# Optimization experiments

Hardware: AMD Instinct MI355X
Metric: run time of the kernel (lower is better)

Reference implementation:

```python
import jax, jax.numpy as jnp
import numpy as np

WD, WH, WW = 6, 6, 6
NUM_HEADS = 8
EPS = 1e-5


def setup_inputs() -> dict:
    key = jax.random.key(0)
    ks = jax.random.split(key, 4)
    B, C, D, H, W = 1, 128, 48, 48, 48
    return {
        "q_map": jax.random.normal(ks[0], (B, C, D, H, W), dtype=jnp.float32),
        "k_map": jax.random.normal(ks[1], (B, C, D, H, W), dtype=jnp.float32),
        "v_map": jax.random.normal(ks[2], (B, C, D, H, W), dtype=jnp.float32),
        "gamma_q": jnp.ones((C,), jnp.float32),
        "beta_q": jnp.zeros((C,), jnp.float32),
        "gamma_kv": jnp.ones((C,), jnp.float32),
        "beta_kv": jnp.zeros((C,), jnp.float32),
        "proj_w": jax.random.normal(ks[3], (C, C), dtype=jnp.float32) * (1.0 / np.sqrt(C)),
        "proj_b": jnp.zeros((C,), jnp.float32),
    }


def _layernorm(x, g, b):
    m = jnp.mean(x, axis=-1, keepdims=True)
    v = jnp.mean(jnp.square(x - m), axis=-1, keepdims=True)
    return (x - m) * jax.lax.rsqrt(v + EPS) * g + b


def _window_partition(x):
    # x: (B, D, H, W, C) -> windows: (B*nD*nH*nW, wd*wh*ww, C)
    B, D, H, W, C = x.shape
    pd, ph, pw = (WD - D % WD) % WD, (WH - H % WH) % WH, (WW - W % WW) % WW
    if pd or ph or pw:
        x = jnp.pad(x, ((0, 0), (0, pd), (0, ph), (0, pw), (0, 0)))
    Dp, Hp, Wp = D + pd, H + ph, W + pw
    x = x.reshape(B, Dp // WD, WD, Hp // WH, WH, Wp // WW, WW, C)
    x = jnp.transpose(x, (0, 1, 3, 5, 2, 4, 6, 7))
    return x.reshape(-1, WD * WH * WW, C), (D, H, W, Dp, Hp, Wp)


def _window_reverse(windows, meta):
    D, H, W, Dp, Hp, Wp = meta
    C = windows.shape[-1]
    nD, nH, nW = Dp // WD, Hp // WH, Wp // WW
    B = windows.shape[0] // (nD * nH * nW)
    x = windows.reshape(B, nD, nH, nW, WD, WH, WW, C)
    x = jnp.transpose(x, (0, 1, 4, 2, 5, 3, 6, 7)).reshape(B, Dp, Hp, Wp, C)
    return x[:, :D, :H, :W, :]


def reference(q_map, k_map, v_map, gamma_q, beta_q, gamma_kv, beta_kv, proj_w, proj_b):
    # (B, C, D, H, W) -> (B, D, H, W, C)
    q_map = jnp.transpose(q_map, (0, 2, 3, 4, 1))
    k_map = jnp.transpose(k_map, (0, 2, 3, 4, 1))
    v_map = jnp.transpose(v_map, (0, 2, 3, 4, 1))

    q, meta = _window_partition(q_map)
    k, _ = _window_partition(k_map)
    v, _ = _window_partition(v_map)

    q = _layernorm(q, gamma_q, beta_q)
    k = _layernorm(k, gamma_kv, beta_kv)
    v = _layernorm(v, gamma_kv, beta_kv)

    Bw, Nq, C = q.shape
    dh = C // NUM_HEADS
    q = q.reshape(Bw, Nq, NUM_HEADS, dh)
    k = k.reshape(Bw, -1, NUM_HEADS, dh)
    v = v.reshape(Bw, -1, NUM_HEADS, dh)

    scale = 1.0 / np.sqrt(dh).astype(np.float32)
    scores = jnp.einsum("bqhd,bkhd->bhqk", q, k) * scale  # (Bw, h, Nq, Nk)
    attn = jax.nn.softmax(scores, axis=-1)
    out = jnp.einsum("bhqk,bkhd->bqhd", attn, v).reshape(Bw, Nq, C)

    out = out @ proj_w.T + proj_b
    out = _window_reverse(out, meta)
    return jnp.transpose(out, (0, 4, 1, 2, 3))  # (B, C, D, H, W)
```

## Files before the change

### kernel.cpp

```cpp
#include <hip/hip_runtime.h>
#include <hip/hip_bf16.h>

typedef short s16x8 __attribute__((ext_vector_type(8)));
typedef float f32x2 __attribute__((ext_vector_type(2)));
typedef float f32x4 __attribute__((ext_vector_type(4)));
typedef float f32x16 __attribute__((ext_vector_type(16)));
typedef unsigned int u32;
typedef unsigned short u16;
typedef u32 u32x4v __attribute__((ext_vector_type(4)));

#define TOK 216
#define T1 448
#define SP 110592
#define BUF0 0
#define VOFF 57344
#define WOFF 122880
#define GBOFF 155648
#define LDS_OLD 157696
#define VHOFF 28672
#define TENB 28311552ull
#define WSNEED (3ull*TENB + 32768ull)
#define QSCALE 0.360673760f

__device__ __forceinline__ u32 pack2(float a, float b) {
  u16 lo = __builtin_bit_cast(u16, __float2bfloat16(a));
  u16 hi = __builtin_bit_cast(u16, __float2bfloat16(b));
  return (u32)lo | ((u32)hi << 16);
}
__device__ __forceinline__ int swz(int row, int inner) {
  return inner ^ ((row & 7) << 4);
}
__device__ __forceinline__ void gload16(const void* g, void* l) {
  __builtin_amdgcn_global_load_lds(
      (const __attribute__((address_space(1))) void*)g,
      (__attribute__((address_space(3))) void*)l, 16, 0, 0);
}

__device__ __forceinline__ void ln_stats(const f32x2* xv, float& mA, float& rA,
                                         float& mB, float& rB) {
  float sA = 0.f, s2A = 0.f, sB = 0.f, s2B = 0.f;
#pragma unroll
  for (int c = 0; c < 32; ++c) {
    sA += xv[c].x; s2A += xv[c].x * xv[c].x;
    sB += xv[c].y; s2B += xv[c].y * xv[c].y;
  }
  sA += __shfl_xor(sA, 1); s2A += __shfl_xor(s2A, 1);
  sB += __shfl_xor(sB, 1); s2B += __shfl_xor(s2B, 1);
  sA += __shfl_xor(sA, 2); s2A += __shfl_xor(s2A, 2);
  sB += __shfl_xor(sB, 2); s2B += __shfl_xor(s2B, 2);
  mA = sA * (1.0f / 128.0f);
  rA = rsqrtf(s2A * (1.0f / 128.0f) - mA * mA + 1e-5f);
  mB = sB * (1.0f / 128.0f);
  rB = rsqrtf(s2B * (1.0f / 128.0f) - mB * mB + 1e-5f);
}

template<bool MASK>
__device__ __forceinline__ void attn_stepH(const char* smem, int jloc, int kt,
                                           s16x8 qfh, int lane,
                                           f32x16& acc, float& lsum) {
  const int half = lane >> 5;
  const int krow = kt * 32 + (lane & 31);
  s16x8 kf = *(const s16x8*)(smem + krow * 128 +
                             ((jloc * 32 + half * 16) ^ ((krow & 7) << 4)));
  f32x16 st = __builtin_amdgcn_mfma_f32_32x32x16_bf16(kf, qfh, (f32x16){}, 0, 0, 0);
  const int vrow = jloc * 16 + (lane & 15);
  s16x8 vf0 = *(const s16x8*)(smem + VHOFF + vrow * 512 +
                              ((kt * 64 + half * 16) ^ ((vrow & 7) << 4)));
  s16x8 vf1 = *(const s16x8*)(smem + VHOFF + vrow * 512 +
                              ((kt * 64 + 32 + half * 16) ^ ((vrow & 7) << 4)));
  const int NR = MASK ? 12 : 16;
  u32 A[8];
  float ts0 = 0.f, ts1 = 0.f;
#pragma unroll
  for (int i = 0; i < 8; ++i) {
    float p0 = (2 * i < NR) ? __builtin_amdgcn_exp2f(st[2 * i]) : 0.f;
    float p1 = (2 * i + 1 < NR) ? __builtin_amdgcn_exp2f(st[2 * i + 1]) : 0.f;
    if (i & 1) ts1 += p0 + p1; else ts0 += p0 + p1;
    A[i] = pack2(p0, p1);
  }
  lsum += ts0 + ts1;
  s16x8 pf0 = __builtin_bit_cast(s16x8, (u32x4v){A[0], A[1], A[2], A[3]});
  s16x8 pf1 = __builtin_bit_cast(s16x8, (u32x4v){A[4], A[5], A[6], A[7]});
  acc = __builtin_amdgcn_mfma_f32_32x32x16_bf16(vf0, pf0, acc, 0, 0, 0);
  acc = __builtin_amdgcn_mfma_f32_32x32x16_bf16(vf1, pf1, acc, 0, 0, 0);
}

template<bool MASK>
__device__ __forceinline__ void attn_stepF(const char* smem, int h, int kt,
                                           s16x8 qfh, int lane,
                                           f32x16& acc, float& lsum) {
  const int half = lane >> 5;
  const int krow = kt * 32 + (lane & 31);
  s16x8 kf = *(const s16x8*)(smem + BUF0 + krow * 256 +
                             swz(krow, h * 32 + half * 16));
  f32x16 st = __builtin_amdgcn_mfma_f32_32x32x16_bf16(kf, qfh, (f32x16){}, 0, 0, 0);
  const int vrow = h * 16 + (lane & 15);
  s16x8 vf0 = *(const s16x8*)(smem + VOFF + vrow * 512 +
                              swz(vrow, kt * 64 + half * 16));
  s16x8 vf1 = *(const s16x8*)(smem + VOFF + vrow * 512 +
                              swz(vrow, kt * 64 + 32 + half * 16));
  const int NR = MASK ? 12 : 16;
  u32 A[8];
  float ts0 = 0.f, ts1 = 0.f;
#pragma unroll
  for (int i = 0; i < 8; ++i) {
    float p0 = (2 * i < NR) ? __builtin_amdgcn_exp2f(st[2 * i]) : 0.f;
    float p1 = (2 * i + 1 < NR) ? __builtin_amdgcn_exp2f(st[2 * i + 1]) : 0.f;
    if (i & 1) ts1 += p0 + p1; else ts0 += p0 + p1;
    A[i] = pack2(p0, p1);
  }
  lsum += ts0 + ts1;
  s16x8 pf0 = __builtin_bit_cast(s16x8, (u32x4v){A[0], A[1], A[2], A[3]});
  s16x8 pf1 = __builtin_bit_cast(s16x8, (u32x4v){A[4], A[5], A[6], A[7]});
  acc = __builtin_amdgcn_mfma_f32_32x32x16_bf16(vf0, pf0, acc, 0, 0, 0);
  acc = __builtin_amdgcn_mfma_f32_32x32x16_bf16(vf1, pf1, acc, 0, 0, 0);
}

extern "C" __global__ __launch_bounds__(256)
void lnpre_kernel(const float* __restrict__ qm, const float* __restrict__ km,
                  const float* __restrict__ vm,
                  const float* __restrict__ gq, const float* __restrict__ bq,
                  const float* __restrict__ gkv, const float* __restrict__ bkv,
                  const float* __restrict__ pw,
                  u16* __restrict__ qn, u16* __restrict__ kn,
                  u16* __restrict__ vn, u16* __restrict__ wbf) {
  const int tid = threadIdx.x;
  const int bid = blockIdx.x;
  if (bid >= 6912) {
#pragma unroll
    for (int k = 0; k < 32; ++k) {
      int idx = tid + 256 * k;
      f32x2 w2 = *(const f32x2*)(pw + idx * 2);
      ((u32*)wbf)[idx] = pack2(w2.x, w2.y);
    }
    return;
  }
  __shared__ __align__(16) float lf[6144];
  __shared__ float gl[128], bl[128];
  const int t = bid / 2304, idx = bid - t * 2304;
  const float* src = t == 0 ? qm : (t == 1 ? km : vm);
  u16* dst = t == 0 ? qn : (t == 1 ? kn : vn);
  const float* gsrc = (t == 0) ? gq : gkv;
  const float* bsrc = (t == 0) ? bq : bkv;
  const float scale = (t == 0) ? QSCALE : 1.0f;
  const int d = idx / 48, h = idx - d * 48;
  const int dh = d * 2304 + h * 48;
  const int lane = tid & 63, wv = tid >> 6;

  if (tid < 128) { gl[tid] = gsrc[tid]; bl[tid] = bsrc[tid]; }
  for (int uu = wv; uu < 24; uu += 4) {
    int j = uu * 64 + lane;
    int ch = j / 12, wq = j - ch * 12;
    gload16(src + (long)ch * SP + dh + wq * 4, (char*)lf + uu * 1024);
  }
  __syncthreads();

  if (tid < 192) {
    const int w = tid >> 2, q = tid & 3;
    float s = 0.f, s2 = 0.f;
#pragma unroll
    for (int c = 0; c < 32; ++c) {
      float x = lf[(q + 4 * c) * 48 + w];
      s += x; s2 += x * x;
    }
    s += __shfl_xor(s, 1); s2 += __shfl_xor(s2, 1);
    s += __shfl_xor(s, 2); s2 += __shfl_xor(s2, 2);
    float m = s * (1.f / 128.f);
    float r = rsqrtf(s2 * (1.f / 128.f) - m * m + 1e-5f);
    u32x4v* op = (u32x4v*)(dst + (long)(dh + w) * 128 + 32 * q);
#pragma unroll
    for (int v4 = 0; v4 < 4; ++v4) {
      u32x4v pk;
#pragma unroll
      for (int e = 0; e < 4; ++e) {
        int ch = 32 * q + v4 * 8 + 2 * e;
        float y0 = ((lf[ch * 48 + w] - m) * r * gl[ch] + bl[ch]) * scale;
        float y1 = ((lf[(ch + 1) * 48 + w] - m) * r * gl[ch + 1] + bl[ch + 1]) * scale;
        pk[e] = pack2(y0, y1);
      }
      op[v4] = pk;
    }
  }
}

extern "C" __global__ __launch_bounds__(448, 4)
void attnh_kernel(u16* __restrict__ qn, const u16* __restrict__ kn,
                  const u16* __restrict__ vn) {
  __shared__ __align__(16) char smem[61440];
  const int tid = threadIdx.x, lane = tid & 63, wv = tid >> 6;
  const int half = lane >> 5;
  const int bid = blockIdx.x;
  const int wid = bid >> 1, hg = bid & 1;
  const int wd6 = (wid >> 6) * 6, wh6 = ((wid >> 3) & 7) * 6, ww6 = (wid & 7) * 6;

  for (int uu = wv; uu < 27; uu += 7) {
    int row = 8 * uu + (lane >> 3);
    int tq = row / 6;
    int g = (wd6 + tq / 6) * 2304 + (wh6 + tq % 6) * 48 + ww6 + row % 6;
    gload16(kn + g * 128 + hg * 64 + (((lane & 7) ^ (row & 7)) << 3),
            smem + uu * 1024);
  }
  for (int uu = wv; uu < 27; uu += 7) {
    int row = 8 * uu + (lane >> 3);
    int tq = row / 6;
    int g = (wd6 + tq / 6) * 2304 + (wh6 + tq % 6) * 48 + ww6 + row % 6;
    gload16(vn + g * 128 + hg * 64 + ((lane & 7) << 3),
            smem + VHOFF + uu * 1024);
  }
  int qrow = wv * 32 + (lane & 31);
  if (qrow > 215) qrow = 215;
  int qtq = qrow / 6;
  int qg = (wd6 + qtq / 6) * 2304 + (wh6 + qtq % 6) * 48 + ww6 + qrow % 6;
  s16x8 qf[4];
#pragma unroll
  for (int j = 0; j < 4; ++j)
    qf[j] = *(const s16x8*)(qn + qg * 128 + (hg * 4 + j) * 16 + half * 8);
  __syncthreads();

  u32 tr[16];
#pragma unroll
  for (int k = 0; k < 8; ++k) {
    int u = tid + 448 * k;
    if (u < 3456) {
      int t = (u >> 5) * 2, c2 = u & 31;
      tr[2 * k]     = *(const u32*)(smem + VHOFF + t * 128 + c2 * 4);
      tr[2 * k + 1] = *(const u32*)(smem + VHOFF + t * 128 + 128 + c2 * 4);
    }
  }
  __syncthreads();
#pragma unroll
  for (int k = 0; k < 8; ++k) {
    int u = tid + 448 * k;
    if (u < 3456) {
      int t = (u >> 5) * 2, c2 = u & 31;
      int st = (t & ~12) | ((t & 4) << 1) | ((t & 8) >> 1);
      int c = 2 * c2;
      u32 w0 = (tr[2 * k] & 0xFFFFu) | (tr[2 * k + 1] << 16);
      u32 w1 = (tr[2 * k] >> 16) | (tr[2 * k + 1] & 0xFFFF0000u);
      *(u32*)(smem + VHOFF + c * 512 + ((st * 2) ^ ((c & 7) << 4))) = w0;
      *(u32*)(smem + VHOFF + (c + 1) * 512 + ((st * 2) ^ (((c + 1) & 7) << 4))) = w1;
    }
  }
  if (tid < 64) {
    int x = (tid & 7) << 4;
    *(u32*)(smem + VHOFF + tid * 512 + (424 ^ x)) = 0;
    *(u32*)(smem + VHOFF + tid * 512 + (428 ^ x)) = 0;
    *(u32*)(smem + VHOFF + tid * 512 + (440 ^ x)) = 0;
    *(u32*)(smem + VHOFF + tid * 512 + (444 ^ x)) = 0;
  }
  __syncthreads();

  u32 oPk[4][4];
#pragma unroll
  for (int hp = 0; hp < 2; ++hp) {
    const int j0 = 2 * hp, j1 = j0 + 1;
    f32x16 a0 = {}, a1 = {};
    float l0 = 0.f, l1 = 0.f;
#pragma unroll 2
    for (int kt = 0; kt < 6; ++kt) {
      attn_stepH<false>(smem, j0, kt, qf[j0], lane, a0, l0);
      attn_stepH<false>(smem, j1, kt, qf[j1], lane, a1, l1);
    }
    attn_stepH<true>(smem, j0, 6, qf[j0], lane, a0, l0);
    attn_stepH<true>(smem, j1, 6, qf[j1], lane, a1, l1);
    l0 += __shfl_xor(l0, 32);
    l1 += __shfl_xor(l1, 32);
    float i0 = 1.0f / l0, i1 = 1.0f / l1;
#pragma unroll
    for (int r = 0; r < 4; ++r) {
      oPk[j0][r] = pack2(a0[2 * r] * i0, a0[2 * r + 1] * i0);
      oPk[j1][r] = pack2(a1[2 * r] * i1, a1[2 * r + 1] * i1);
    }
  }
  __syncthreads();

  {
    const int tok = wv * 32 + (lane & 31);
#pragma unroll
    for (int j = 0; j < 4; ++j) {
      int chb = j * 32 + half * 8;
      *(u32*)(smem + tok * 128 + ((chb)      ^ ((tok & 7) << 4))) = oPk[j][0];
      *(u32*)(smem + tok * 128 + ((chb + 4)  ^ ((tok & 7) << 4))) = oPk[j][1];
      *(u32*)(smem + tok * 128 + ((chb + 16) ^ ((tok & 7) << 4))) = oPk[j][2];
      *(u32*)(smem + tok * 128 + ((chb + 20) ^ ((tok & 7) << 4))) = oPk[j][3];
    }
  }
  __syncthreads();

#pragma unroll
  for (int it = 0; it < 4; ++it) {
    int i = tid + 448 * it;
    int row = i >> 3;
    if (row < 216) {
      int chunk = i & 7;
      f32x4 v = *(const f32x4*)(smem + row * 128 +
                                ((chunk * 16) ^ ((row & 7) << 4)));
      int tq = row / 6;
      int g = (wd6 + tq / 6) * 2304 + (wh6 + tq % 6) * 48 + ww6 + row % 6;
      *(f32x4*)(qn + g * 128 + hg * 64 + chunk * 8) = v;
    }
  }
}

extern "C" __global__ __launch_bounds__(256, 3)
void proj_kernel(const u16* __restrict__ on, const u16* __restrict__ wbf,
                 const float* __restrict__ pb, float* __restrict__ out) {
  __shared__ __align__(16) char smem[45056];
  const int tid = threadIdx.x, lane = tid & 63, wv = tid >> 6;
  const int bid = blockIdx.x;
  const int dh = (bid / 48) * 2304 + (bid % 48) * 48;
  for (int uu = wv; uu < 32; uu += 4) {
    int row = 4 * uu + (lane >> 4);
    gload16(wbf + row * 128 + (((lane & 15) ^ (row & 15)) << 3),
            smem + uu * 1024);
  }
  for (int uu = wv; uu < 12; uu += 4) {
    int row = 4 * uu + (lane >> 4);
    gload16(on + (long)(dh + row) * 128 + (((lane & 15) ^ (row & 15)) << 3),
            smem + 32768 + uu * 1024);
  }
  __syncthreads();
#pragma unroll
  for (int jj = 0; jj < 2; ++jj) {
    int jt = wv * 2 + jj;
    int rw = jt * 16 + (lane & 15);
    s16x8 af[4];
#pragma unroll
    for (int kk = 0; kk < 4; ++kk)
      af[kk] = *(const s16x8*)(smem + rw * 256 +
                               ((kk * 64 + (lane >> 4) * 16) ^ ((rw & 15) << 4)));
    f32x4 pbv = *(const f32x4*)(pb + jt * 16 + (lane >> 4) * 4);
#pragma unroll
    for (int t = 0; t < 3; ++t) {
      int tok = t * 16 + (lane & 15);
      f32x4 acc = {};
#pragma unroll
      for (int kk = 0; kk < 4; ++kk) {
        s16x8 bfr = *(const s16x8*)(smem + 32768 + tok * 256 +
                                    ((kk * 64 + (lane >> 4) * 16) ^ ((tok & 15) << 4)));
        acc = __builtin_amdgcn_mfma_f32_16x16x32_bf16(af[kk], bfr, acc, 0, 0, 0);
      }
#pragma unroll
      for (int r = 0; r < 4; ++r) {
        int j = jt * 16 + (lane >> 4) * 4 + r;
        out[(long)j * SP + dh + tok] = acc[r] + pbv[r];
      }
    }
  }
}

extern "C" __global__ __launch_bounds__(T1, 2)
void ca3d_kernel(const float* __restrict__ qm, const float* __restrict__ km,
                 const float* __restrict__ vm,
                 const float* __restrict__ gq, const float* __restrict__ bq,
                 const float* __restrict__ gkv, const float* __restrict__ bkv,
                 const float* __restrict__ pw, const float* __restrict__ pb,
                 float* __restrict__ out) {
  extern __shared__ __align__(16) char smem[];
  const int tid = threadIdx.x;
  const int lane = tid & 63;
  const int wv = tid >> 6;
  const int bid = blockIdx.x;
  const int wid = ((bid & 7) << 6) | (bid >> 3);
  const int wd = wid >> 6, wh = (wid >> 3) & 7, ww = wid & 7;
  const int boff = wd * 6 * 2304 + wh * 6 * 48 + ww * 6;

  for (int i = tid * 16; i < VOFF + 65536; i += T1 * 16)
    *(f32x4*)(smem + i) = (f32x4){};
  if (tid < 128) {
    ((float*)(smem + GBOFF))[tid] = gq[tid];
    ((float*)(smem + GBOFF + 512))[tid] = bq[tid];
    ((float*)(smem + GBOFF + 1024))[tid] = gkv[tid];
    ((float*)(smem + GBOFF + 1536))[tid] = bkv[tid];
  }
  const bool lnAct = tid < 432;
  const int tp = tid >> 2;
  const int cbase = (tid & 3) * 32;
  const int tA = tp * 2, tB = tA + 1;
  int td = tA / 36, tr_ = tA - td * 36;
  int th_ = tr_ / 6, tw_ = tr_ - th_ * 6;
  const int gpos = boff + td * 2304 + th_ * 48 + tw_;
  const int vposA = (tA & ~0xC) | ((tA & 4) << 1) | ((tA & 8) >> 1);

  f32x2 qv[32], kv[32], vv[32];
  if (lnAct) {
#pragma unroll
    for (int c = 0; c < 32; ++c)
      qv[c] = *(const f32x2*)(qm + gpos + (cbase + c) * SP);
#pragma unroll
    for (int c = 0; c < 32; ++c)
      kv[c] = *(const f32x2*)(km + gpos + (cbase + c) * SP);
  }
  __syncthreads();
  const float* gql = (const float*)(smem + GBOFF);
  const float* bql = (const float*)(smem + GBOFF + 512);
  const float* gkl = (const float*)(smem + GBOFF + 1024);
  const float* bkl = (const float*)(smem + GBOFF + 1536);
  if (lnAct) {
    float mA, rA, mB, rB;
    ln_stats(qv, mA, rA, mB, rB);
#pragma unroll
    for (int c = 0; c < 32; c += 2) {
      int cc = cbase + c;
      float g0 = gql[cc], g1 = gql[cc + 1], b0 = bql[cc], b1 = bql[cc + 1];
      *(u32*)(smem + BUF0 + tA * 256 + swz(tA, cc * 2)) =
          pack2(((qv[c].x - mA) * rA * g0 + b0) * QSCALE,
                ((qv[c + 1].x - mA) * rA * g1 + b1) * QSCALE);
      *(u32*)(smem + BUF0 + tB * 256 + swz(tB, cc * 2)) =
          pack2(((qv[c].y - mB) * rB * g0 + b0) * QSCALE,
                ((qv[c + 1].y - mB) * rB * g1 + b1) * QSCALE);
    }
#pragma unroll
    for (int c = 0; c < 32; ++c)
      vv[c] = *(const f32x2*)(vm + gpos + (cbase + c) * SP);
  }
  __syncthreads();
  s16x8 qf[8];
  {
    int row = wv * 32 + (lane & 31);
    int ib = (lane >> 5) * 16;
#pragma unroll
    for (int h = 0; h < 8; ++h)
      qf[h] = *(const s16x8*)(smem + BUF0 + row * 256 + swz(row, h * 32 + ib));
  }
  __syncthreads();
  if (lnAct) {
    {
      float mA, rA, mB, rB;
      ln_stats(kv, mA, rA, mB, rB);
#pragma unroll
      for (int c = 0; c < 32; c += 2) {
        int cc = cbase + c;
        float g0 = gkl[cc], g1 = gkl[cc + 1], b0 = bkl[cc], b1 = bkl[cc + 1];
        *(u32*)(smem + BUF0 + tA * 256 + swz(tA, cc * 2)) =
            pack2((kv[c].x - mA) * rA * g0 + b0,
                  (kv[c + 1].x - mA) * rA * g1 + b1);
        *(u32*)(smem + BUF0 + tB * 256 + swz(tB, cc * 2)) =
            pack2((kv[c].y - mB) * rB * g0 + b0,
                  (kv[c + 1].y - mB) * rB * g1 + b1);
      }
    }
    {
      float mA, rA, mB, rB;
      ln_stats(vv, mA, rA, mB, rB);
#pragma unroll
      for (int c = 0; c < 32; ++c) {
        int cc = cbase + c;
        float g0 = gkl[cc], b0 = bkl[cc];
        *(u32*)(smem + VOFF + cc * 512 + swz(cc, vposA * 2)) =
            pack2((vv[c].x - mA) * rA * g0 + b0,
                  (vv[c].y - mB) * rB * g0 + b0);
      }
    }
  }
  for (int i = tid; i < 8192; i += T1) {
    int j = i >> 6, c2 = i & 63;
    f32x2 w2 = *(const f32x2*)(pw + j * 128 + c2 * 2);
    *(u32*)(smem + WOFF + j * 256 + swz(j, c2 * 4)) = pack2(w2.x, w2.y);
  }
  __syncthreads();
  u32 oPk[8][4];
#pragma unroll
  for (int hp = 0; hp < 4; ++hp) {
    const int h0 = hp * 2, h1 = h0 + 1;
    f32x16 a0 = {}, a1 = {};
    float l0 = 0.f, l1 = 0.f;
#pragma unroll 1
    for (int kt = 0; kt < 6; ++kt) {
      attn_stepF<false>(smem, h0, kt, qf[h0], lane, a0, l0);
      attn_stepF<false>(smem, h1, kt, qf[h1], lane, a1, l1);
    }
    attn_stepF<true>(smem, h0, 6, qf[h0], lane, a0, l0);
    attn_stepF<true>(smem, h1, 6, qf[h1], lane, a1, l1);
    l0 += __shfl_xor(l0, 32);
    l1 += __shfl_xor(l1, 32);
    float i0 = 1.0f / l0, i1 = 1.0f / l1;
#pragma unroll
    for (int r = 0; r < 4; ++r) {
      oPk[h0][r] = pack2(a0[2 * r] * i0, a0[2 * r + 1] * i0);
      oPk[h1][r] = pack2(a1[2 * r] * i1, a1[2 * r + 1] * i1);
    }
  }
  __syncthreads();
  {
    const int tok = wv * 32 + (lane & 31);
    const int half = lane >> 5;
#pragma unroll
    for (int h = 0; h < 8; ++h) {
      int chb = h * 32 + half * 8;
      *(u32*)(smem + BUF0 + tok * 256 + swz(tok, chb))      = oPk[h][0];
      *(u32*)(smem + BUF0 + tok * 256 + swz(tok, chb + 4))  = oPk[h][1];
      *(u32*)(smem + BUF0 + tok * 256 + swz(tok, chb + 16)) = oPk[h][2];
      *(u32*)(smem + BUF0 + tok * 256 + swz(tok, chb + 20)) = oPk[h][3];
    }
  }
  __syncthreads();
#pragma unroll 1
  for (int ti = 0; ti < 2; ++ti) {
    int tt = wv * 2 + ti;
    int tok = tt * 16 + (lane & 15);
    s16x8 bfr[4];
#pragma unroll
    for (int kk = 0; kk < 4; ++kk)
      bfr[kk] = *(const s16x8*)(smem + BUF0 + tok * 256 +
                                swz(tok, kk * 64 + (lane >> 4) * 16));
    bool tokValid = tok < TOK;
    int tdd = tok / 36, trr = tok - tdd * 36;
    int thh = trr / 6, tww = trr - thh * 6;
    int pos = boff + tdd * 2304 + thh * 48 + tww;
#pragma unroll 1
    for (int jt = 0; jt < 8; ++jt) {
      f32x4 acc = {};
#pragma unroll
      for (int kk = 0; kk < 4; ++kk) {
        int rw = jt * 16 + (lane & 15);
        s16x8 af = *(const s16x8*)(smem + WOFF + rw * 256 +
                                   swz(rw, kk * 64 + (lane >> 4) * 16));
        acc = __builtin_amdgcn_mfma_f32_16x16x32_bf16(af, bfr[kk], acc, 0, 0, 0);
      }
      f32x4 pbv = *(const f32x4*)(pb + jt * 16 + (lane >> 4) * 4);
      if (tokValid) {
#pragma unroll
        for (int r = 0; r < 4; ++r) {
          int j = jt * 16 + (lane >> 4) * 4 + r;
          out[j * SP + pos] = acc[r] + pbv[r];
        }
      }
    }
  }
}

extern "C" void kernel_launch(void* const* d_in, const int* in_sizes, int n_in,
                              void* d_out, int out_size, void* d_ws, size_t ws_size,
                              hipStream_t stream) {
  const float* qm  = (const float*)d_in[0];
  const float* km  = (const float*)d_in[1];
  const float* vm  = (const float*)d_in[2];
  const float* gq  = (const float*)d_in[3];
  const float* bq  = (const float*)d_in[4];
  const float* gkv = (const float*)d_in[5];
  const float* bkv = (const float*)d_in[6];
  const float* pw  = (const float*)d_in[7];
  const float* pb  = (const float*)d_in[8];
  if (ws_size >= WSNEED) {
    u16* qn  = (u16*)d_ws;
    u16* kn  = (u16*)((char*)d_ws + TENB);
    u16* vn  = (u16*)((char*)d_ws + 2 * TENB);
    u16* wbf = (u16*)((char*)d_ws + 3 * TENB);
    hipLaunchKernelGGL(lnpre_kernel, dim3(6913), dim3(256), 0, stream,
                       qm, km, vm, gq, bq, gkv, bkv, pw, qn, kn, vn, wbf);
    hipLaunchKernelGGL(attnh_kernel, dim3(1024), dim3(448), 0, stream,
                       qn, kn, vn);
    hipLaunchKernelGGL(proj_kernel, dim3(2304), dim3(256), 0, stream,
                       qn, wbf, pb, (float*)d_out);
  } else {
    hipLaunchKernelGGL(ca3d_kernel, dim3(512), dim3(T1), LDS_OLD, stream,
                       qm, km, vm, gq, bq, gkv, bkv, pw, pb, (float*)d_out);
  }
}
```

Baseline: 137.0 us.

## Restructure layernorm prepass to per-token register reduction with swizzled LDS transpose

The layernorm prepass is rewritten so that each wave owns 64 consecutive tokens and each lane reduces one token across all 128 channels directly from global memory, replacing the cooperative LDS staging and cross-lane shuffle reduction. The normalized values are packed to bf16, written to a per-wave XOR-swizzled LDS tile, and then stored coalesced in token-major layout. Block count and size drop to 2593 blocks of 128 threads. The input is read twice (once for the statistics, once for normalization), which relies on cache hits and trades extra load traffic for simpler indexing and fewer barriers.

```diff
diff --git a/kernel.cpp b/kernel.cpp
--- a/kernel.cpp
+++ b/kernel.cpp
@@ -116,7 +116,7 @@
   acc = __builtin_amdgcn_mfma_f32_32x32x16_bf16(vf1, pf1, acc, 0, 0, 0);
 }
 
-extern "C" __global__ __launch_bounds__(256)
+extern "C" __global__ __launch_bounds__(128)
 void lnpre_kernel(const float* __restrict__ qm, const float* __restrict__ km,
                   const float* __restrict__ vm,
                   const float* __restrict__ gq, const float* __restrict__ bq,
@@ -126,60 +126,63 @@
                   u16* __restrict__ vn, u16* __restrict__ wbf) {
   const int tid = threadIdx.x;
   const int bid = blockIdx.x;
-  if (bid >= 6912) {
-#pragma unroll
-    for (int k = 0; k < 32; ++k) {
-      int idx = tid + 256 * k;
+  if (bid >= 2592) {
+#pragma unroll
+    for (int k = 0; k < 64; ++k) {
+      int idx = tid + 128 * k;
       f32x2 w2 = *(const f32x2*)(pw + idx * 2);
       ((u32*)wbf)[idx] = pack2(w2.x, w2.y);
     }
     return;
   }
-  __shared__ __align__(16) float lf[6144];
-  __shared__ float gl[128], bl[128];
-  const int t = bid / 2304, idx = bid - t * 2304;
+  __shared__ __align__(16) char lds[32768];
+  const int lane = tid & 63, wv = tid >> 6;
+  const int t = bid / 864, rb = bid - t * 864;
   const float* src = t == 0 ? qm : (t == 1 ? km : vm);
   u16* dst = t == 0 ? qn : (t == 1 ? kn : vn);
-  const float* gsrc = (t == 0) ? gq : gkv;
-  const float* bsrc = (t == 0) ? bq : bkv;
+  const float* g = (t == 0) ? gq : gkv;
+  const float* b = (t == 0) ? bq : bkv;
   const float scale = (t == 0) ? QSCALE : 1.0f;
-  const int d = idx / 48, h = idx - d * 48;
-  const int dh = d * 2304 + h * 48;
-  const int lane = tid & 63, wv = tid >> 6;
-
-  if (tid < 128) { gl[tid] = gsrc[tid]; bl[tid] = bsrc[tid]; }
-  for (int uu = wv; uu < 24; uu += 4) {
-    int j = uu * 64 + lane;
-    int ch = j / 12, wq = j - ch * 12;
-    gload16(src + (long)ch * SP + dh + wq * 4, (char*)lf + uu * 1024);
-  }
-  __syncthreads();
-
-  if (tid < 192) {
-    const int w = tid >> 2, q = tid & 3;
-    float s = 0.f, s2 = 0.f;
-#pragma unroll
-    for (int c = 0; c < 32; ++c) {
-      float x = lf[(q + 4 * c) * 48 + w];
-      s += x; s2 += x * x;
-    }
-    s += __shfl_xor(s, 1); s2 += __shfl_xor(s2, 1);
-    s += __shfl_xor(s, 2); s2 += __shfl_xor(s2, 2);
-    float m = s * (1.f / 128.f);
-    float r = rsqrtf(s2 * (1.f / 128.f) - m * m + 1e-5f);
-    u32x4v* op = (u32x4v*)(dst + (long)(dh + w) * 128 + 32 * q);
-#pragma unroll
-    for (int v4 = 0; v4 < 4; ++v4) {
-      u32x4v pk;
-#pragma unroll
-      for (int e = 0; e < 4; ++e) {
-        int ch = 32 * q + v4 * 8 + 2 * e;
-        float y0 = ((lf[ch * 48 + w] - m) * r * gl[ch] + bl[ch]) * scale;
-        float y1 = ((lf[(ch + 1) * 48 + w] - m) * r * gl[ch + 1] + bl[ch + 1]) * scale;
-        pk[e] = pack2(y0, y1);
-      }
-      op[v4] = pk;
-    }
+  const long T0 = (long)(rb * 2 + wv) * 64;
+  const float* base = src + T0 + lane;
+
+  float s0 = 0.f, s1 = 0.f, s2 = 0.f, s3 = 0.f;
+  float q0 = 0.f, q1 = 0.f, q2 = 0.f, q3 = 0.f;
+#pragma unroll 8
+  for (int c = 0; c < 128; c += 4) {
+    float x0 = base[(long)(c + 0) * SP];
+    float x1 = base[(long)(c + 1) * SP];
+    float x2 = base[(long)(c + 2) * SP];
+    float x3 = base[(long)(c + 3) * SP];
+    s0 += x0; q0 += x0 * x0; s1 += x1; q1 += x1 * x1;
+    s2 += x2; q2 += x2 * x2; s3 += x3; q3 += x3 * x3;
+  }
+  float s = (s0 + s1) + (s2 + s3);
+  float sq = (q0 + q1) + (q2 + q3);
+  float m = s * (1.f / 128.f);
+  float r = rsqrtf(sq * (1.f / 128.f) - m * m + 1e-5f);
+  asm volatile("" ::: "memory");
+
+  char* lw = lds + wv * 16384;
+#pragma unroll 4
+  for (int ch8 = 0; ch8 < 16; ++ch8) {
+    u32x4v pk;
+#pragma unroll
+    for (int e = 0; e < 4; ++e) {
+      int c = ch8 * 8 + e * 2;
+      float x0 = base[(long)c * SP];
+      float x1 = base[(long)(c + 1) * SP];
+      pk[e] = pack2(((x0 - m) * r * g[c] + b[c]) * scale,
+                    ((x1 - m) * r * g[c + 1] + b[c + 1]) * scale);
+    }
+    *(u32x4v*)(lw + lane * 256 + ((ch8 ^ (lane & 15)) << 4)) = pk;
+  }
+#pragma unroll 4
+  for (int it = 0; it < 16; ++it) {
+    int row = it * 4 + (lane >> 4);
+    int cc = lane & 15;
+    u32x4v v = *(const u32x4v*)(lw + row * 256 + ((cc ^ (row & 15)) << 4));
+    *(u32x4v*)(dst + (T0 + row) * 128 + cc * 8) = v;
   }
 }
 
@@ -547,7 +550,7 @@
     u16* kn  = (u16*)((char*)d_ws + TENB);
     u16* vn  = (u16*)((char*)d_ws + 2 * TENB);
     u16* wbf = (u16*)((char*)d_ws + 3 * TENB);
-    hipLaunchKernelGGL(lnpre_kernel, dim3(6913), dim3(256), 0, stream,
+    hipLaunchKernelGGL(lnpre_kernel, dim3(2593), dim3(128), 0, stream,
                        qm, km, vm, gq, bq, gkv, bkv, pw, qn, kn, vn, wbf);
     hipLaunchKernelGGL(attnh_kernel, dim3(1024), dim3(448), 0, stream,
                        qn, kn, vn);
```

New measurement: 140.3 us. +2.4%, slower.
